# Kernel tuning notes

Measured on AMD Instinct MI355X. Metric: run time of the kernel, lower is better.

Reference implementation:

```python
import jax, jax.numpy as jnp
import numpy as np

B, T, N, F, H, HEADS = 4, 10, 2048, 64, 128, 4
D = H // HEADS
E = 65536
NTOT = B * N


def setup_inputs() -> dict:
    key = jax.random.key(0)
    ks = jax.random.split(key, 16)
    s = 0.05
    return {
        "x": jax.random.normal(ks[0], (B, T, N, F), jnp.float32),
        "W": jax.random.normal(ks[1], (F, H), jnp.float32) * s,
        "att_src": jax.random.normal(ks[2], (HEADS, D), jnp.float32) * s,
        "att_dst": jax.random.normal(ks[3], (HEADS, D), jnp.float32) * s,
        "gat_bias": jnp.zeros((H,), jnp.float32),
        "W_ih0": jax.random.normal(ks[4], (4 * H, H), jnp.float32) * s,
        "W_hh0": jax.random.normal(ks[5], (4 * H, H), jnp.float32) * s,
        "b_ih0": jnp.zeros((4 * H,), jnp.float32),
        "b_hh0": jnp.zeros((4 * H,), jnp.float32),
        "W_ih1": jax.random.normal(ks[6], (4 * H, H), jnp.float32) * s,
        "W_hh1": jax.random.normal(ks[7], (4 * H, H), jnp.float32) * s,
        "b_ih1": jnp.zeros((4 * H,), jnp.float32),
        "b_hh1": jnp.zeros((4 * H,), jnp.float32),
        "ln_gamma": jnp.ones((H,), jnp.float32),
        "ln_beta": jnp.zeros((H,), jnp.float32),
        "edge_index": jax.random.randint(ks[8], (2, E), 0, NTOT, dtype=jnp.int32),
    }


def reference(x, W, att_src, att_dst, gat_bias,
              W_ih0, W_hh0, b_ih0, b_hh0,
              W_ih1, W_hh1, b_ih1, b_hh1,
              ln_gamma, ln_beta, edge_index):
    # ---- GAT spatial encoding, vectorized over all T timesteps ----
    loops = jnp.arange(NTOT, dtype=edge_index.dtype)  # PyG GATConv adds self-loops
    src = jnp.concatenate([edge_index[0], loops])
    dst = jnp.concatenate([edge_index[1], loops])

    x_flat = x.transpose(1, 0, 2, 3).reshape(T, NTOT, F)          # [T, B*N, F]
    h = (x_flat @ W).reshape(T, NTOT, HEADS, D)                    # per-head projections
    a_src = jnp.einsum('tnhd,hd->tnh', h, att_src)                 # [T, NTOT, HEADS]
    a_dst = jnp.einsum('tnhd,hd->tnh', h, att_dst)
    e = jax.nn.leaky_relu(a_src[:, src] + a_dst[:, dst], 0.2)      # [T, Ef, HEADS]

    def seg_softmax(e_t):
        m = jax.ops.segment_max(e_t, dst, num_segments=NTOT)
        ex = jnp.exp(e_t - m[dst])
        den = jax.ops.segment_sum(ex, dst, num_segments=NTOT)
        return ex / den[dst]

    alpha = jax.vmap(seg_softmax)(e)                               # edge softmax per target
    msg = alpha[..., None] * h[:, src]                             # [T, Ef, HEADS, D]
    agg = jax.vmap(lambda m: jax.ops.segment_sum(m, dst, num_segments=NTOT))(msg)
    spatial = jax.nn.relu(agg.reshape(T, NTOT, H) + gat_bias)      # concat heads + bias + relu

    # ---- 2-layer LSTM over time (batched over all B*N node sequences) ----
    def step(carry, xt):
        h0, c0, h1, c1 = carry
        g0 = xt @ W_ih0.T + h0 @ W_hh0.T + (b_ih0 + b_hh0)
        i, f, g, o = jnp.split(g0, 4, axis=-1)
        c0 = jax.nn.sigmoid(f) * c0 + jax.nn.sigmoid(i) * jnp.tanh(g)
        h0 = jax.nn.sigmoid(o) * jnp.tanh(c0)
        g1 = h0 @ W_ih1.T + h1 @ W_hh1.T + (b_ih1 + b_hh1)
        i, f, g, o = jnp.split(g1, 4, axis=-1)
        c1 = jax.nn.sigmoid(f) * c1 + jax.nn.sigmoid(i) * jnp.tanh(g)
        h1 = jax.nn.sigmoid(o) * jnp.tanh(c1)
        return (h0, c0, h1, c1), None

    z = jnp.zeros((NTOT, H), spatial.dtype)
    (_, _, h1, _), _ = jax.lax.scan(step, (z, z, z, z), spatial)
    ctx = h1.reshape(B, N, H)

    # ---- LayerNorm ----
    mu = ctx.mean(-1, keepdims=True)
    var = ctx.var(-1, keepdims=True)
    return (ctx - mu) / jnp.sqrt(var + 1e-5) * ln_gamma + ln_beta
```

## Files before the change

### kernel.cpp

```cpp
#include <hip/hip_runtime.h>

#define T_ 10
#define B_ 4
#define N_ 2048
#define NTOT 8192
#define F_ 64
#define H_ 128
#define NHEADS 4
#define D_ 32
#define E_ 65536
#define EF 73728
#define HPAD 136

typedef __bf16 bf16x8 __attribute__((ext_vector_type(8)));
typedef float f32x4 __attribute__((ext_vector_type(4)));
typedef unsigned short u16;

__device__ __forceinline__ float bf2f(u16 u){
  union { unsigned int i; float f; } v; v.i = ((unsigned int)u) << 16; return v.f;
}
__device__ __forceinline__ u16 f2bf(float f){
  union { float f; unsigned int i; } v; v.f = f;
  return (u16)((v.i + 0x7FFFu + ((v.i >> 16) & 1u)) >> 16);
}
__device__ __forceinline__ float rcpf(float x){ return __builtin_amdgcn_rcpf(x); }
__device__ __forceinline__ float sigf(float x){ return rcpf(1.f + __expf(-x)); }
__device__ __forceinline__ float tanhfast(float x){ return 1.f - 2.f * rcpf(__expf(2.f * x) + 1.f); }
__device__ __forceinline__ float lrelu(float x){ return x > 0.f ? x : 0.2f * x; }

__global__ __launch_bounds__(256) void k_init(int* __restrict__ cnt){
  int i = blockIdx.x * 256 + threadIdx.x;
  if(i < NTOT) cnt[i] = 0;
}

__global__ __launch_bounds__(256) void k_count(const int* __restrict__ ei, int* __restrict__ cnt){
  int e = blockIdx.x * 256 + threadIdx.x;
  if(e < E_) atomicAdd(&cnt[ei[E_ + e]], 1);
}

__global__ __launch_bounds__(1024) void k_scan(const int* __restrict__ cnt,
                                               int* __restrict__ rowst,
                                               int* __restrict__ cursor){
  __shared__ int lds[1024];
  const int t = threadIdx.x;
  int loc[8];
  int s = 0;
  #pragma unroll
  for(int i = 0; i < 8; i++){ loc[i] = s; s += cnt[t * 8 + i]; }
  lds[t] = s;
  __syncthreads();
  for(int off = 1; off < 1024; off <<= 1){
    int v = lds[t];
    int a = (t >= off) ? lds[t - off] : 0;
    __syncthreads();
    lds[t] = v + a;
    __syncthreads();
  }
  const int base = (t > 0) ? lds[t - 1] : 0;
  #pragma unroll
  for(int i = 0; i < 8; i++){
    rowst[t * 8 + i] = base + loc[i];
    cursor[t * 8 + i] = 0;
  }
  if(t == 1023) rowst[NTOT] = lds[1023];
}

__global__ __launch_bounds__(256) void k_fill(const int* __restrict__ ei,
                                              const int* __restrict__ rowst,
                                              int* __restrict__ cursor,
                                              int* __restrict__ csr,
                                              int* __restrict__ csr_dst){
  int e = blockIdx.x * 256 + threadIdx.x;
  if(e < E_){
    int d = ei[E_ + e];
    int pos = atomicAdd(&cursor[d], 1);
    csr[rowst[d] + pos] = ei[e];
    csr_dst[rowst[d] + pos] = d;
  }
}

__global__ __launch_bounds__(256) void k_wconv(const float* __restrict__ s0, u16* __restrict__ d0,
                                               const float* __restrict__ s1, u16* __restrict__ d1,
                                               const float* __restrict__ s2, u16* __restrict__ d2,
                                               const float* __restrict__ s3, u16* __restrict__ d3,
                                               const float* __restrict__ W, u16* __restrict__ Wt){
  int i = blockIdx.x * 256 + threadIdx.x;
  if(blockIdx.y == 4){
    if(i < H_ * F_){
      int nn = i >> 6, f = i & 63;
      Wt[i] = f2bf(W[f * H_ + nn]);
    }
    return;
  }
  const float* src = blockIdx.y == 0 ? s0 : blockIdx.y == 1 ? s1 : blockIdx.y == 2 ? s2 : s3;
  u16* dst = blockIdx.y == 0 ? d0 : blockIdx.y == 1 ? d1 : blockIdx.y == 2 ? d2 : d3;
  if(i < 512 * 128){
    int p = i >> 7, k = i & 127;
    int w = p >> 6, g = (p >> 4) & 3, l = p & 15;
    int row = g * 128 + w * 16 + l;
    dst[i] = f2bf(src[row * 128 + k]);
  }
}

__global__ __launch_bounds__(256) void k_projm(const float* __restrict__ x,
    const u16* __restrict__ Wt, const float* __restrict__ att_s, const float* __restrict__ att_d,
    u16* __restrict__ hbuf, float* __restrict__ asrc, float* __restrict__ adst){
  const int tid  = threadIdx.x;
  const int wave = tid >> 6;
  const int lane = tid & 63;
  const int l15  = lane & 15;
  const int quad = lane >> 4;
  const int r0   = blockIdx.x * 64 + wave * 16;
  const int row  = r0 + l15;
  const int t = row >> 13, nt = row & 8191;
  const int b = nt >> 11, n = nt & 2047;
  const float* xrow = x + (((size_t)b * T_ + t) * N_ + n) * F_;

  bf16x8 a[2];
  #pragma unroll
  for(int ks = 0; ks < 2; ks++){
    const float4 f0 = *(const float4*)(xrow + ks * 32 + quad * 8);
    const float4 f1 = *(const float4*)(xrow + ks * 32 + quad * 8 + 4);
    bf16x8 av;
    av[0] = (__bf16)f0.x; av[1] = (__bf16)f0.y; av[2] = (__bf16)f0.z; av[3] = (__bf16)f0.w;
    av[4] = (__bf16)f1.x; av[5] = (__bf16)f1.y; av[6] = (__bf16)f1.z; av[7] = (__bf16)f1.w;
    a[ks] = av;
  }

  f32x4 acc[8];
  #pragma unroll
  for(int c = 0; c < 8; c++){ f32x4 z = {0.f,0.f,0.f,0.f}; acc[c] = z; }
  #pragma unroll
  for(int c = 0; c < 8; c++){
    #pragma unroll
    for(int ks = 0; ks < 2; ks++){
      const bf16x8 bv = *(const bf16x8*)(Wt + (c * 16 + l15) * F_ + ks * 32 + quad * 8);
      acc[c] = __builtin_amdgcn_mfma_f32_16x16x32_bf16(a[ks], bv, acc[c], 0, 0, 0);
    }
  }

  float ps[4][4], pd[4][4];
  #pragma unroll
  for(int r = 0; r < 4; r++)
    #pragma unroll
    for(int h = 0; h < 4; h++){ ps[r][h] = 0.f; pd[r][h] = 0.f; }

  #pragma unroll
  for(int c = 0; c < 8; c++){
    const int col = c * 16 + l15;
    const float asv = att_s[col];
    const float adv = att_d[col];
    const int head = c >> 1;
    #pragma unroll
    for(int r = 0; r < 4; r++){
      const float v = acc[c][r];
      hbuf[(size_t)(r0 + quad * 4 + r) * H_ + col] = f2bf(v);
      ps[r][head] += v * asv;
      pd[r][head] += v * adv;
    }
  }
  #pragma unroll
  for(int m = 8; m >= 1; m >>= 1){
    #pragma unroll
    for(int r = 0; r < 4; r++)
      #pragma unroll
      for(int h = 0; h < 4; h++){
        ps[r][h] += __shfl_xor(ps[r][h], m);
        pd[r][h] += __shfl_xor(pd[r][h], m);
      }
  }
  if(l15 == 0){
    #pragma unroll
    for(int r = 0; r < 4; r++){
      const int rw = r0 + quad * 4 + r;
      #pragma unroll
      for(int h = 0; h < 4; h++){
        asrc[(size_t)rw * NHEADS + h] = ps[r][h];
        adst[(size_t)rw * NHEADS + h] = pd[r][h];
      }
    }
  }
}

__global__ __launch_bounds__(256) void k_mden(const float* __restrict__ asrc,
    const float* __restrict__ adst, const int* __restrict__ rowst, const int* __restrict__ csr,
    float* __restrict__ m_, float* __restrict__ den_){
  const int gid = blockIdx.x * 256 + threadIdx.x;
  const int head = gid & 3;
  const int node = (gid >> 2) & 8191;
  const int t = gid >> 15;
  const int rbase = t * NTOT;
  const float ad = adst[(size_t)(rbase + node) * NHEADS + head];
  float m = lrelu(asrc[(size_t)(rbase + node) * NHEADS + head] + ad);
  float den = 1.f;
  const int rs = rowst[node], re = rowst[node + 1];
  for(int i = rs; i < re; i++){
    const int s = csr[i];
    const float ev = lrelu(asrc[(size_t)(rbase + s) * NHEADS + head] + ad);
    const float nm = fmaxf(m, ev);
    den = den * __expf(m - nm) + __expf(ev - nm);
    m = nm;
  }
  m_[gid] = m;
  den_[gid] = den;
}

__global__ __launch_bounds__(256) void k_alpha(const float* __restrict__ asrc,
    const float* __restrict__ adst, const int* __restrict__ csr, const int* __restrict__ csr_dst,
    const float* __restrict__ m_, const float* __restrict__ den_, float* __restrict__ alphaC){
  const int p = blockIdx.x * 256 + threadIdx.x;
  const int t = blockIdx.y;
  const int rbase = t * NTOT;
  int s, d;
  if(p < E_){ s = csr[p]; d = csr_dst[p]; } else { s = d = p - E_; }
  const float4 as4 = *(const float4*)&asrc[(size_t)(rbase + s) * NHEADS];
  const float4 ad4 = *(const float4*)&adst[(size_t)(rbase + d) * NHEADS];
  const float4 m4  = *(const float4*)&m_[(size_t)(rbase + d) * NHEADS];
  const float4 dn4 = *(const float4*)&den_[(size_t)(rbase + d) * NHEADS];
  float4 o;
  o.x = __expf(lrelu(as4.x + ad4.x) - m4.x) * rcpf(dn4.x);
  o.y = __expf(lrelu(as4.y + ad4.y) - m4.y) * rcpf(dn4.y);
  o.z = __expf(lrelu(as4.z + ad4.z) - m4.z) * rcpf(dn4.z);
  o.w = __expf(lrelu(as4.w + ad4.w) - m4.w) * rcpf(dn4.w);
  *(float4*)&alphaC[((size_t)t * EF + p) * NHEADS] = o;
}

__global__ __launch_bounds__(256) void k_agg(const u16* __restrict__ hbuf,
    const float* __restrict__ alphaC, const int* __restrict__ rowst, const int* __restrict__ csr,
    const float* __restrict__ gbias, u16* __restrict__ spat){
  const int tid = threadIdx.x;
  const int wave = tid >> 6;
  const int lane = tid & 63;
  const int task = blockIdx.x * 4 + wave;
  const int node = task & 8191;
  const int t = task >> 13;
  const int rbase = t * NTOT;
  const int d0 = lane, d1 = lane + 64;

  const float4 aself = *(const float4*)&alphaC[((size_t)t * EF + E_ + node) * NHEADS];
  float acc0 = (lane < 32 ? aself.x : aself.y) * bf2f(hbuf[(size_t)(rbase + node) * H_ + d0]);
  float acc1 = (lane < 32 ? aself.z : aself.w) * bf2f(hbuf[(size_t)(rbase + node) * H_ + d1]);
  const int rs = rowst[node], re = rowst[node + 1];
  for(int i = rs; i < re; i++){
    const int s = csr[i];
    const float4 av = *(const float4*)&alphaC[((size_t)t * EF + i) * NHEADS];
    const float a0 = lane < 32 ? av.x : av.y;
    const float a1 = lane < 32 ? av.z : av.w;
    acc0 += a0 * bf2f(hbuf[(size_t)(rbase + s) * H_ + d0]);
    acc1 += a1 * bf2f(hbuf[(size_t)(rbase + s) * H_ + d1]);
  }
  const float v0 = acc0 + gbias[d0];
  const float v1 = acc1 + gbias[d1];
  spat[(size_t)(rbase + node) * H_ + d0] = f2bf(v0 > 0.f ? v0 : 0.f);
  spat[(size_t)(rbase + node) * H_ + d1] = f2bf(v1 > 0.f ? v1 : 0.f);
}

__global__ __launch_bounds__(512) __attribute__((amdgpu_waves_per_eu(2, 2))) void k_lstm(
    const u16* __restrict__ spat,
    const u16* __restrict__ Wp_ih0, const u16* __restrict__ Wp_hh0,
    const float* __restrict__ bih0, const float* __restrict__ bhh0,
    const u16* __restrict__ Wp_ih1, const u16* __restrict__ Wp_hh1,
    const float* __restrict__ bih1, const float* __restrict__ bhh1,
    const float* __restrict__ lng, const float* __restrict__ lnb,
    float* __restrict__ out)
{
  __shared__ __align__(16) u16 xin[32 * HPAD];
  __shared__ __align__(16) u16 h0s[2][32 * HPAD];
  __shared__ __align__(16) u16 h1s[2][32 * HPAD];
  __shared__ __align__(16) float hfin[32 * 129];

  const int tid  = threadIdx.x;
  const int wave = tid >> 6;
  const int lane = tid & 63;
  const int l15  = lane & 15;
  const int quad = lane >> 4;
  const int n0   = blockIdx.x * 32;
  const int dim  = wave * 16 + l15;

  for(int i = tid; i < 2 * 32 * HPAD; i += 512){
    ((u16*)h0s)[i] = 0; ((u16*)h1s)[i] = 0;
  }
  {
    const u16* src = spat + (size_t)n0 * H_;
    const int r = tid >> 4, c = tid & 15;
    *(uint4*)(xin + r * HPAD + c * 8) = *(const uint4*)(src + r * 128 + c * 8);
  }
  float cst[16];
  #pragma unroll
  for(int i = 0; i < 16; i++) cst[i] = 0.f;

  float bias[2][4];
  #pragma unroll
  for(int g = 0; g < 4; g++){
    bias[0][g] = bih0[g * 128 + dim] + bhh0[g * 128 + dim];
    bias[1][g] = bih1[g * 128 + dim] + bhh1[g * 128 + dim];
  }

  const size_t fbase = (size_t)(wave * 64 + l15) * 128 + quad * 8;
  bf16x8 whh[2][4][4];
  #pragma unroll
  for(int nt = 0; nt < 4; nt++){
    #pragma unroll
    for(int ks = 0; ks < 4; ks++){
      const size_t o = fbase + (size_t)nt * 16 * 128 + ks * 32;
      whh[0][nt][ks] = *(const bf16x8*)(Wp_hh0 + o);
      whh[1][nt][ks] = *(const bf16x8*)(Wp_hh1 + o);
    }
  }
  __syncthreads();

  #pragma unroll 1
  for(int t = 0; t < T_; t++){
    const int rp = t & 1, wp = rp ^ 1;
    #pragma unroll
    for(int layer = 0; layer < 2; layer++){
      const u16* Wih = layer ? Wp_ih1 : Wp_ih0;
      const u16* xp  = layer ? h0s[wp] : xin;
      const u16* hp  = layer ? h1s[rp] : h0s[rp];

      bf16x8 wih[4][4];
      #pragma unroll
      for(int nt = 0; nt < 4; nt++){
        #pragma unroll
        for(int ks = 0; ks < 4; ks++)
          wih[nt][ks] = *(const bf16x8*)(Wih + fbase + (size_t)nt * 16 * 128 + ks * 32);
      }

      f32x4 acc[2][4];
      #pragma unroll
      for(int nt = 0; nt < 4; nt++){
        const float bv = bias[layer][nt];
        f32x4 b4 = {bv, bv, bv, bv};
        acc[0][nt] = b4; acc[1][nt] = b4;
      }

      #pragma unroll
      for(int ks = 0; ks < 4; ks++){
        const int ka = ks * 32 + quad * 8;
        const bf16x8 a0 = *(const bf16x8*)(xp + l15 * HPAD + ka);
        const bf16x8 a1 = *(const bf16x8*)(xp + (16 + l15) * HPAD + ka);
        #pragma unroll
        for(int nt = 0; nt < 4; nt++){
          acc[0][nt] = __builtin_amdgcn_mfma_f32_16x16x32_bf16(a0, wih[nt][ks], acc[0][nt], 0, 0, 0);
          acc[1][nt] = __builtin_amdgcn_mfma_f32_16x16x32_bf16(a1, wih[nt][ks], acc[1][nt], 0, 0, 0);
        }
      }

      #pragma unroll
      for(int ks = 0; ks < 4; ks++){
        const int ka = ks * 32 + quad * 8;
        const bf16x8 a0 = *(const bf16x8*)(hp + l15 * HPAD + ka);
        const bf16x8 a1 = *(const bf16x8*)(hp + (16 + l15) * HPAD + ka);
        #pragma unroll
        for(int nt = 0; nt < 4; nt++){
          const bf16x8 b = whh[layer][nt][ks];
          acc[0][nt] = __builtin_amdgcn_mfma_f32_16x16x32_bf16(a0, b, acc[0][nt], 0, 0, 0);
          acc[1][nt] = __builtin_amdgcn_mfma_f32_16x16x32_bf16(a1, b, acc[1][nt], 0, 0, 0);
        }
      }

      u16* hcur = layer ? h1s[wp] : h0s[wp];
      #pragma unroll
      for(int mt = 0; mt < 2; mt++){
        #pragma unroll
        for(int r = 0; r < 4; r++){
          const int node = mt * 16 + quad * 4 + r;
          const float gi = acc[mt][0][r];
          const float gf = acc[mt][1][r];
          const float gg = acc[mt][2][r];
          const float go = acc[mt][3][r];
          const int ci = layer * 8 + mt * 4 + r;
          const float c = sigf(gf) * cst[ci] + sigf(gi) * tanhfast(gg);
          cst[ci] = c;
          const float hv = sigf(go) * tanhfast(c);
          hcur[node * HPAD + dim] = f2bf(hv);
          if(layer == 1 && t == T_ - 1)
            hfin[node * 129 + dim] = hv;
        }
      }
      if(layer == 1 && t < T_ - 1){
        const u16* src = spat + (size_t)((t + 1) * NTOT + n0) * H_;
        const int r = tid >> 4, c = tid & 15;
        *(uint4*)(xin + r * HPAD + c * 8) = *(const uint4*)(src + r * 128 + c * 8);
      }
      __syncthreads();
    }
  }

  {
    const int node = tid >> 4;
    const int c0 = (tid & 15) * 8;
    float v[8];
    #pragma unroll
    for(int j = 0; j < 8; j++) v[j] = hfin[node * 129 + c0 + j];
    float s = 0.f;
    #pragma unroll
    for(int j = 0; j < 8; j++) s += v[j];
    #pragma unroll
    for(int m = 8; m >= 1; m >>= 1) s += __shfl_xor(s, m);
    const float mu = s * (1.f / H_);
    float q = 0.f;
    #pragma unroll
    for(int j = 0; j < 8; j++){ const float d = v[j] - mu; q += d * d; }
    #pragma unroll
    for(int m = 8; m >= 1; m >>= 1) q += __shfl_xor(q, m);
    const float rstd = rsqrtf(q * (1.f / H_) + 1e-5f);
    #pragma unroll
    for(int j = 0; j < 8; j++)
      out[(size_t)(n0 + node) * H_ + c0 + j] = (v[j] - mu) * rstd * lng[c0 + j] + lnb[c0 + j];
  }
}

extern "C" void kernel_launch(void* const* d_in, const int* in_sizes, int n_in,
                              void* d_out, int out_size, void* d_ws, size_t ws_size,
                              hipStream_t stream) {
  (void)in_sizes; (void)n_in; (void)out_size; (void)ws_size;
  const float* x     = (const float*)d_in[0];
  const float* W     = (const float*)d_in[1];
  const float* att_s = (const float*)d_in[2];
  const float* att_d = (const float*)d_in[3];
  const float* gbias = (const float*)d_in[4];
  const float* Wih0  = (const float*)d_in[5];
  const float* Whh0  = (const float*)d_in[6];
  const float* bih0  = (const float*)d_in[7];
  const float* bhh0  = (const float*)d_in[8];
  const float* Wih1  = (const float*)d_in[9];
  const float* Whh1  = (const float*)d_in[10];
  const float* bih1  = (const float*)d_in[11];
  const float* bhh1  = (const float*)d_in[12];
  const float* lng   = (const float*)d_in[13];
  const float* lnb   = (const float*)d_in[14];
  const int*   ei    = (const int*)d_in[15];
  float* out = (float*)d_out;

  char* p = (char*)d_ws;
  auto carve = [&](size_t bytes) -> void* {
    void* r = (void*)p;
    p += (bytes + 255) & ~(size_t)255;
    return r;
  };
  u16* Wp_ih0 = (u16*)carve(512 * 128 * 2);
  u16* Wp_hh0 = (u16*)carve(512 * 128 * 2);
  u16* Wp_ih1 = (u16*)carve(512 * 128 * 2);
  u16* Wp_hh1 = (u16*)carve(512 * 128 * 2);
  u16* Wt     = (u16*)carve(H_ * F_ * 2);
  u16*   hbuf   = (u16*)carve((size_t)T_ * NTOT * H_ * 2);
  float* asrc   = (float*)carve((size_t)T_ * NTOT * NHEADS * 4);
  float* adst   = (float*)carve((size_t)T_ * NTOT * NHEADS * 4);
  float* m_     = (float*)carve((size_t)T_ * NTOT * NHEADS * 4);
  float* den_   = (float*)carve((size_t)T_ * NTOT * NHEADS * 4);
  float* alphaC = (float*)carve((size_t)T_ * EF * NHEADS * 4);
  u16*   spat   = (u16*)carve((size_t)T_ * NTOT * H_ * 2);
  int*   cnt    = (int*)carve(NTOT * 4);
  int*   curs   = (int*)carve(NTOT * 4);
  int*   rowst  = (int*)carve((NTOT + 1) * 4);
  int*   csr    = (int*)carve((size_t)E_ * 4);
  int*   csrd   = (int*)carve((size_t)E_ * 4);

  hipLaunchKernelGGL(k_init,  dim3(32),        dim3(256),  0, stream, cnt);
  hipLaunchKernelGGL(k_count, dim3(256),       dim3(256),  0, stream, ei, cnt);
  hipLaunchKernelGGL(k_scan,  dim3(1),         dim3(1024), 0, stream, cnt, rowst, curs);
  hipLaunchKernelGGL(k_fill,  dim3(256),       dim3(256),  0, stream, ei, rowst, curs, csr, csrd);
  hipLaunchKernelGGL(k_wconv, dim3(256, 5),    dim3(256),  0, stream,
                     Wih0, Wp_ih0, Whh0, Wp_hh0, Wih1, Wp_ih1, Whh1, Wp_hh1, W, Wt);
  hipLaunchKernelGGL(k_projm, dim3(1280),      dim3(256),  0, stream, x, Wt, att_s, att_d, hbuf, asrc, adst);
  hipLaunchKernelGGL(k_mden,  dim3(1280),      dim3(256),  0, stream, asrc, adst, rowst, csr, m_, den_);
  hipLaunchKernelGGL(k_alpha, dim3(288, 10),   dim3(256),  0, stream, asrc, adst, csr, csrd, m_, den_, alphaC);
  hipLaunchKernelGGL(k_agg,   dim3(20480),     dim3(256),  0, stream, hbuf, alphaC, rowst, csr, gbias, spat);
  hipLaunchKernelGGL(k_lstm,  dim3(256),       dim3(512),  0, stream, spat,
                     Wp_ih0, Wp_hh0, bih0, bhh0, Wp_ih1, Wp_hh1, bih1, bhh1, lng, lnb, out);
}
```

Measured before the change: 351.2 us.

## Halve LSTM node tile and stream weights from L2 instead of registers

The LSTM kernel now handles 16 nodes per block instead of 32 and launches 512 blocks, so twice as many blocks spread across the GPU's compute units. Recurrent weights are no longer cached in registers. Both input and recurrent weights are now streamed from global memory in double-buffered chunks of four per k-slice, and the fixed waves-per-EU attribute is dropped. This cuts register pressure and raises parallelism. In exchange, every block reloads all weights on every timestep and layer, and each weight fragment feeds half as many MFMAs.

```diff
diff --git a/kernel.cpp b/kernel.cpp
--- a/kernel.cpp
+++ b/kernel.cpp
@@ -255,7 +255,7 @@
   spat[(size_t)(rbase + node) * H_ + d1] = f2bf(v1 > 0.f ? v1 : 0.f);
 }
 
-__global__ __launch_bounds__(512) __attribute__((amdgpu_waves_per_eu(2, 2))) void k_lstm(
+__global__ __launch_bounds__(512) void k_lstm(
     const u16* __restrict__ spat,
     const u16* __restrict__ Wp_ih0, const u16* __restrict__ Wp_hh0,
     const float* __restrict__ bih0, const float* __restrict__ bhh0,
@@ -264,30 +264,30 @@
     const float* __restrict__ lng, const float* __restrict__ lnb,
     float* __restrict__ out)
 {
-  __shared__ __align__(16) u16 xin[32 * HPAD];
-  __shared__ __align__(16) u16 h0s[2][32 * HPAD];
-  __shared__ __align__(16) u16 h1s[2][32 * HPAD];
-  __shared__ __align__(16) float hfin[32 * 129];
+  __shared__ __align__(16) u16 xin[16 * HPAD];
+  __shared__ __align__(16) u16 h0s[2][16 * HPAD];
+  __shared__ __align__(16) u16 h1s[2][16 * HPAD];
+  __shared__ __align__(16) float hfin[16 * 129];
 
   const int tid  = threadIdx.x;
   const int wave = tid >> 6;
   const int lane = tid & 63;
   const int l15  = lane & 15;
   const int quad = lane >> 4;
-  const int n0   = blockIdx.x * 32;
+  const int n0   = blockIdx.x * 16;
   const int dim  = wave * 16 + l15;
 
-  for(int i = tid; i < 2 * 32 * HPAD; i += 512){
+  for(int i = tid; i < 2 * 16 * HPAD; i += 512){
     ((u16*)h0s)[i] = 0; ((u16*)h1s)[i] = 0;
   }
-  {
+  if(tid < 256){
     const u16* src = spat + (size_t)n0 * H_;
     const int r = tid >> 4, c = tid & 15;
     *(uint4*)(xin + r * HPAD + c * 8) = *(const uint4*)(src + r * 128 + c * 8);
   }
-  float cst[16];
-  #pragma unroll
-  for(int i = 0; i < 16; i++) cst[i] = 0.f;
+  float cst[8];
+  #pragma unroll
+  for(int i = 0; i < 8; i++) cst[i] = 0.f;
 
   float bias[2][4];
   #pragma unroll
@@ -295,19 +295,9 @@
     bias[0][g] = bih0[g * 128 + dim] + bhh0[g * 128 + dim];
     bias[1][g] = bih1[g * 128 + dim] + bhh1[g * 128 + dim];
   }
+  __syncthreads();
 
   const size_t fbase = (size_t)(wave * 64 + l15) * 128 + quad * 8;
-  bf16x8 whh[2][4][4];
-  #pragma unroll
-  for(int nt = 0; nt < 4; nt++){
-    #pragma unroll
-    for(int ks = 0; ks < 4; ks++){
-      const size_t o = fbase + (size_t)nt * 16 * 128 + ks * 32;
-      whh[0][nt][ks] = *(const bf16x8*)(Wp_hh0 + o);
-      whh[1][nt][ks] = *(const bf16x8*)(Wp_hh1 + o);
-    }
-  }
-  __syncthreads();
 
   #pragma unroll 1
   for(int t = 0; t < T_; t++){
@@ -315,70 +305,74 @@
     #pragma unroll
     for(int layer = 0; layer < 2; layer++){
       const u16* Wih = layer ? Wp_ih1 : Wp_ih0;
+      const u16* Whh = layer ? Wp_hh1 : Wp_hh0;
       const u16* xp  = layer ? h0s[wp] : xin;
       const u16* hp  = layer ? h1s[rp] : h0s[rp];
 
-      bf16x8 wih[4][4];
-      #pragma unroll
-      for(int nt = 0; nt < 4; nt++){
-        #pragma unroll
-        for(int ks = 0; ks < 4; ks++)
-          wih[nt][ks] = *(const bf16x8*)(Wih + fbase + (size_t)nt * 16 * 128 + ks * 32);
-      }
-
-      f32x4 acc[2][4];
+      f32x4 acc[4];
       #pragma unroll
       for(int nt = 0; nt < 4; nt++){
         const float bv = bias[layer][nt];
         f32x4 b4 = {bv, bv, bv, bv};
-        acc[0][nt] = b4; acc[1][nt] = b4;
+        acc[nt] = b4;
       }
 
-      #pragma unroll
-      for(int ks = 0; ks < 4; ks++){
-        const int ka = ks * 32 + quad * 8;
-        const bf16x8 a0 = *(const bf16x8*)(xp + l15 * HPAD + ka);
-        const bf16x8 a1 = *(const bf16x8*)(xp + (16 + l15) * HPAD + ka);
+      auto half_mm = [&](const u16* Wm, const u16* ap){
+        const u16* WBm = Wm + fbase;
+        bf16x8 wa[4], wb[4];
         #pragma unroll
-        for(int nt = 0; nt < 4; nt++){
-          acc[0][nt] = __builtin_amdgcn_mfma_f32_16x16x32_bf16(a0, wih[nt][ks], acc[0][nt], 0, 0, 0);
-          acc[1][nt] = __builtin_amdgcn_mfma_f32_16x16x32_bf16(a1, wih[nt][ks], acc[1][nt], 0, 0, 0);
+        for(int nt = 0; nt < 4; nt++) wa[nt] = *(const bf16x8*)(WBm + nt * 2048);
+        #pragma unroll
+        for(int nt = 0; nt < 4; nt++) wb[nt] = *(const bf16x8*)(WBm + nt * 2048 + 32);
+        {
+          const bf16x8 a = *(const bf16x8*)(ap + l15 * HPAD + quad * 8);
+          #pragma unroll
+          for(int nt = 0; nt < 4; nt++)
+            acc[nt] = __builtin_amdgcn_mfma_f32_16x16x32_bf16(a, wa[nt], acc[nt], 0, 0, 0);
         }
-      }
-
-      #pragma unroll
-      for(int ks = 0; ks < 4; ks++){
-        const int ka = ks * 32 + quad * 8;
-        const bf16x8 a0 = *(const bf16x8*)(hp + l15 * HPAD + ka);
-        const bf16x8 a1 = *(const bf16x8*)(hp + (16 + l15) * HPAD + ka);
         #pragma unroll
-        for(int nt = 0; nt < 4; nt++){
-          const bf16x8 b = whh[layer][nt][ks];
-          acc[0][nt] = __builtin_amdgcn_mfma_f32_16x16x32_bf16(a0, b, acc[0][nt], 0, 0, 0);
-          acc[1][nt] = __builtin_amdgcn_mfma_f32_16x16x32_bf16(a1, b, acc[1][nt], 0, 0, 0);
+        for(int nt = 0; nt < 4; nt++) wa[nt] = *(const bf16x8*)(WBm + nt * 2048 + 64);
+        {
+          const bf16x8 a = *(const bf16x8*)(ap + l15 * HPAD + 32 + quad * 8);
+          #pragma unroll
+          for(int nt = 0; nt < 4; nt++)
+            acc[nt] = __builtin_amdgcn_mfma_f32_16x16x32_bf16(a, wb[nt], acc[nt], 0, 0, 0);
         }
-      }
+        #pragma unroll
+        for(int nt = 0; nt < 4; nt++) wb[nt] = *(const bf16x8*)(WBm + nt * 2048 + 96);
+        {
+          const bf16x8 a = *(const bf16x8*)(ap + l15 * HPAD + 64 + quad * 8);
+          #pragma unroll
+          for(int nt = 0; nt < 4; nt++)
+            acc[nt] = __builtin_amdgcn_mfma_f32_16x16x32_bf16(a, wa[nt], acc[nt], 0, 0, 0);
+        }
+        {
+          const bf16x8 a = *(const bf16x8*)(ap + l15 * HPAD + 96 + quad * 8);
+          #pragma unroll
+          for(int nt = 0; nt < 4; nt++)
+            acc[nt] = __builtin_amdgcn_mfma_f32_16x16x32_bf16(a, wb[nt], acc[nt], 0, 0, 0);
+        }
+      };
+      half_mm(Wih, xp);
+      half_mm(Whh, hp);
 
       u16* hcur = layer ? h1s[wp] : h0s[wp];
       #pragma unroll
-      for(int mt = 0; mt < 2; mt++){
-        #pragma unroll
-        for(int r = 0; r < 4; r++){
-          const int node = mt * 16 + quad * 4 + r;
-          const float gi = acc[mt][0][r];
-          const float gf = acc[mt][1][r];
-          const float gg = acc[mt][2][r];
-          const float go = acc[mt][3][r];
-          const int ci = layer * 8 + mt * 4 + r;
-          const float c = sigf(gf) * cst[ci] + sigf(gi) * tanhfast(gg);
-          cst[ci] = c;
-          const float hv = sigf(go) * tanhfast(c);
-          hcur[node * HPAD + dim] = f2bf(hv);
-          if(layer == 1 && t == T_ - 1)
-            hfin[node * 129 + dim] = hv;
-        }
+      for(int r = 0; r < 4; r++){
+        const int node = quad * 4 + r;
+        const float gi = acc[0][r];
+        const float gf = acc[1][r];
+        const float gg = acc[2][r];
+        const float go = acc[3][r];
+        const int ci = layer * 4 + r;
+        const float c = sigf(gf) * cst[ci] + sigf(gi) * tanhfast(gg);
+        cst[ci] = c;
+        const float hv = sigf(go) * tanhfast(c);
+        hcur[node * HPAD + dim] = f2bf(hv);
+        if(layer == 1 && t == T_ - 1)
+          hfin[node * 129 + dim] = hv;
       }
-      if(layer == 1 && t < T_ - 1){
+      if(layer == 1 && t < T_ - 1 && tid < 256){
         const u16* src = spat + (size_t)((t + 1) * NTOT + n0) * H_;
         const int r = tid >> 4, c = tid & 15;
         *(uint4*)(xin + r * HPAD + c * 8) = *(const uint4*)(src + r * 128 + c * 8);
@@ -387,7 +381,7 @@
     }
   }
 
-  {
+  if(tid < 256){
     const int node = tid >> 4;
     const int c0 = (tid & 15) * 8;
     float v[8];
@@ -467,6 +461,6 @@
   hipLaunchKernelGGL(k_mden,  dim3(1280),      dim3(256),  0, stream, asrc, adst, rowst, csr, m_, den_);
   hipLaunchKernelGGL(k_alpha, dim3(288, 10),   dim3(256),  0, stream, asrc, adst, csr, csrd, m_, den_, alphaC);
   hipLaunchKernelGGL(k_agg,   dim3(20480),     dim3(256),  0, stream, hbuf, alphaC, rowst, csr, gbias, spat);
-  hipLaunchKernelGGL(k_lstm,  dim3(256),       dim3(512),  0, stream, spat,
+  hipLaunchKernelGGL(k_lstm,  dim3(512),       dim3(512),  0, stream, spat,
                      Wp_ih0, Wp_hh0, bih0, bhh0, Wp_ih1, Wp_hh1, bih1, bhh1, lng, lnb, out);
 }
```

After: 429.1 us. 22.2% more time.

## Stream LSTM weight fragments through double-buffered registers instead of holding them resident

Applied to the files above, without the earlier changes.

Removes the persistent register-resident W_hh fragments and the per-layer 16-fragment W_ih preload. Weights are now streamed from global/L2 in a two-slot register double buffer: the next k-slice loads while MFMAs run on the current one. The waves_per_eu(2,2) attribute is dropped, so the lower register pressure can allow more waves per SIMD. The cost is re-fetching the recurrent weights from cache every layer and timestep, with load latency only partly hidden behind four MFMA pairs per phase.

```diff
diff --git a/kernel.cpp b/kernel.cpp
--- a/kernel.cpp
+++ b/kernel.cpp
@@ -255,7 +255,7 @@
   spat[(size_t)(rbase + node) * H_ + d1] = f2bf(v1 > 0.f ? v1 : 0.f);
 }
 
-__global__ __launch_bounds__(512) __attribute__((amdgpu_waves_per_eu(2, 2))) void k_lstm(
+__global__ __launch_bounds__(512) void k_lstm(
     const u16* __restrict__ spat,
     const u16* __restrict__ Wp_ih0, const u16* __restrict__ Wp_hh0,
     const float* __restrict__ bih0, const float* __restrict__ bhh0,
@@ -295,19 +295,25 @@
     bias[0][g] = bih0[g * 128 + dim] + bhh0[g * 128 + dim];
     bias[1][g] = bih1[g * 128 + dim] + bhh1[g * 128 + dim];
   }
+  __syncthreads();
 
   const size_t fbase = (size_t)(wave * 64 + l15) * 128 + quad * 8;
-  bf16x8 whh[2][4][4];
-  #pragma unroll
-  for(int nt = 0; nt < 4; nt++){
-    #pragma unroll
-    for(int ks = 0; ks < 4; ks++){
-      const size_t o = fbase + (size_t)nt * 16 * 128 + ks * 32;
-      whh[0][nt][ks] = *(const bf16x8*)(Wp_hh0 + o);
-      whh[1][nt][ks] = *(const bf16x8*)(Wp_hh1 + o);
-    }
-  }
-  __syncthreads();
+
+#define PHASE(CUR, NXT, NXTBASE, AP, KA, DOLOAD)                                   \
+  {                                                                                \
+    if(DOLOAD){                                                                    \
+      _Pragma("unroll")                                                            \
+      for(int nt = 0; nt < 4; nt++)                                                \
+        NXT[nt] = *(const bf16x8*)((NXTBASE) + nt * 2048);                         \
+    }                                                                              \
+    const bf16x8 a0 = *(const bf16x8*)((AP) + l15 * HPAD + (KA));                  \
+    const bf16x8 a1 = *(const bf16x8*)((AP) + (16 + l15) * HPAD + (KA));           \
+    _Pragma("unroll")                                                              \
+    for(int nt = 0; nt < 4; nt++){                                                 \
+      acc[0][nt] = __builtin_amdgcn_mfma_f32_16x16x32_bf16(a0, CUR[nt], acc[0][nt], 0, 0, 0); \
+      acc[1][nt] = __builtin_amdgcn_mfma_f32_16x16x32_bf16(a1, CUR[nt], acc[1][nt], 0, 0, 0); \
+    }                                                                              \
+  }
 
   #pragma unroll 1
   for(int t = 0; t < T_; t++){
@@ -315,16 +321,9 @@
     #pragma unroll
     for(int layer = 0; layer < 2; layer++){
       const u16* Wih = layer ? Wp_ih1 : Wp_ih0;
+      const u16* Whh = layer ? Wp_hh1 : Wp_hh0;
       const u16* xp  = layer ? h0s[wp] : xin;
       const u16* hp  = layer ? h1s[rp] : h0s[rp];
-
-      bf16x8 wih[4][4];
-      #pragma unroll
-      for(int nt = 0; nt < 4; nt++){
-        #pragma unroll
-        for(int ks = 0; ks < 4; ks++)
-          wih[nt][ks] = *(const bf16x8*)(Wih + fbase + (size_t)nt * 16 * 128 + ks * 32);
-      }
 
       f32x4 acc[2][4];
       #pragma unroll
@@ -334,30 +333,20 @@
         acc[0][nt] = b4; acc[1][nt] = b4;
       }
 
+      const u16* WihB = Wih + fbase;
+      const u16* WhhB = Whh + fbase;
+      bf16x8 bk0[4], bk1[4];
       #pragma unroll
-      for(int ks = 0; ks < 4; ks++){
-        const int ka = ks * 32 + quad * 8;
-        const bf16x8 a0 = *(const bf16x8*)(xp + l15 * HPAD + ka);
-        const bf16x8 a1 = *(const bf16x8*)(xp + (16 + l15) * HPAD + ka);
-        #pragma unroll
-        for(int nt = 0; nt < 4; nt++){
-          acc[0][nt] = __builtin_amdgcn_mfma_f32_16x16x32_bf16(a0, wih[nt][ks], acc[0][nt], 0, 0, 0);
-          acc[1][nt] = __builtin_amdgcn_mfma_f32_16x16x32_bf16(a1, wih[nt][ks], acc[1][nt], 0, 0, 0);
-        }
-      }
-
-      #pragma unroll
-      for(int ks = 0; ks < 4; ks++){
-        const int ka = ks * 32 + quad * 8;
-        const bf16x8 a0 = *(const bf16x8*)(hp + l15 * HPAD + ka);
-        const bf16x8 a1 = *(const bf16x8*)(hp + (16 + l15) * HPAD + ka);
-        #pragma unroll
-        for(int nt = 0; nt < 4; nt++){
-          const bf16x8 b = whh[layer][nt][ks];
-          acc[0][nt] = __builtin_amdgcn_mfma_f32_16x16x32_bf16(a0, b, acc[0][nt], 0, 0, 0);
-          acc[1][nt] = __builtin_amdgcn_mfma_f32_16x16x32_bf16(a1, b, acc[1][nt], 0, 0, 0);
-        }
-      }
+      for(int nt = 0; nt < 4; nt++) bk0[nt] = *(const bf16x8*)(WihB + nt * 2048);
+
+      PHASE(bk0, bk1, WihB + 32, xp,      quad * 8, 1)
+      PHASE(bk1, bk0, WihB + 64, xp, 32 + quad * 8, 1)
+      PHASE(bk0, bk1, WihB + 96, xp, 64 + quad * 8, 1)
+      PHASE(bk1, bk0, WhhB,      xp, 96 + quad * 8, 1)
+      PHASE(bk0, bk1, WhhB + 32, hp,      quad * 8, 1)
+      PHASE(bk1, bk0, WhhB + 64, hp, 32 + quad * 8, 1)
+      PHASE(bk0, bk1, WhhB + 96, hp, 64 + quad * 8, 1)
+      PHASE(bk1, bk0, WhhB,      hp, 96 + quad * 8, 0)
 
       u16* hcur = layer ? h1s[wp] : h0s[wp];
       #pragma unroll
@@ -386,6 +375,7 @@
       __syncthreads();
     }
   }
+#undef PHASE
 
   {
     const int node = tid >> 4;
```

Result: no change. 356.1 us (+1.4%).
